# Performance work log

Hardware: AMD Instinct MI355X
Metric: run time of the kernel (lower is better)

## Reference

```python
import jax, jax.numpy as jnp
import numpy as np

N_NODES = 50000
N_EDGES = 400000
N_GRAPHS = 64
D_IN = 256
D_HID = 256
D_OUT = 16


def _gcn_conv(x, edge_index, W, b):
    """PyG-style GCNConv: h = D^{-1/2}(A+I)D^{-1/2} (x @ W) + b."""
    n = x.shape[0]
    loop = jnp.arange(n)
    src = jnp.concatenate([edge_index[0], loop])  # [E+N]
    dst = jnp.concatenate([edge_index[1], loop])
    deg = jax.ops.segment_sum(jnp.ones_like(dst, x.dtype), dst, num_segments=n)
    dinv = jnp.where(deg > 0, jax.lax.rsqrt(deg), jnp.zeros_like(deg))
    norm = dinv[src] * dinv[dst]  # [E+N]
    h = x @ W  # linear transform first (as PyG does)
    msg = h[src] * norm[:, None]  # gather + scale, [E+N, D]
    out = jax.ops.segment_sum(msg, dst, num_segments=n)  # scatter-add
    return out + b


def setup_inputs() -> dict:
    key = jax.random.key(0)
    ks = jax.random.split(key, 12)
    x = jax.random.normal(ks[0], (N_NODES, D_IN), dtype=jnp.float32)
    edge_index = jax.random.randint(ks[1], (2, N_EDGES), 0, N_NODES, dtype=jnp.int64)
    batch = jnp.sort(jax.random.randint(ks[2], (N_NODES,), 0, N_GRAPHS, dtype=jnp.int64))

    def glorot(k, fan_in, fan_out):
        s = np.sqrt(6.0 / (fan_in + fan_out)).astype(np.float32)
        return jax.random.uniform(k, (fan_in, fan_out), jnp.float32, -s, s)

    return {
        "x": x,
        "edge_index": edge_index,
        "batch": batch,
        "W1": glorot(ks[3], D_IN, D_HID), "b1": jnp.zeros((D_HID,), jnp.float32),
        "W2": glorot(ks[4], D_HID, D_HID), "b2": jnp.zeros((D_HID,), jnp.float32),
        "W3": glorot(ks[5], D_HID, D_HID), "b3": jnp.zeros((D_HID,), jnp.float32),
        "Wfc": glorot(ks[6], D_HID, D_OUT), "bfc": jnp.zeros((D_OUT,), jnp.float32),
    }


def reference(x, edge_index, batch, W1, b1, W2, b2, W3, b3, Wfc, bfc):
    h = jax.nn.relu(_gcn_conv(x, edge_index, W1, b1))
    h = jax.nn.relu(_gcn_conv(h, edge_index, W2, b2))
    h = jax.nn.relu(_gcn_conv(h, edge_index, W3, b3))
    # global_mean_pool over batch ids
    sums = jax.ops.segment_sum(h, batch, num_segments=N_GRAPHS)  # [G, D]
    cnts = jax.ops.segment_sum(jnp.ones_like(batch, h.dtype), batch, num_segments=N_GRAPHS)
    pooled = sums / jnp.maximum(cnts, 1.0)[:, None]
    return pooled @ Wfc + bfc  # [G, D_OUT]
```

## Files before the change

### kernel.cpp

```cpp
#include <hip/hip_runtime.h>

#define NN 50000
#define NE 400000
#define NG 64
#define D 256
#define DOUT 16

typedef __attribute__((ext_vector_type(8))) _Float16 f16x8;
typedef __attribute__((ext_vector_type(8))) unsigned short u16x8;
typedef __attribute__((ext_vector_type(4))) float f32x4;

__device__ __forceinline__ unsigned short f2h(float x) {
    union { _Float16 h; unsigned short u; } v;
    v.h = (_Float16)x;
    return v.u;
}
__device__ __forceinline__ float h2f(unsigned short u) {
    union { _Float16 h; unsigned short u; } v;
    v.u = u;
    return (float)v.h;
}

__device__ __forceinline__ void async_cp16(void* lds, const void* g) {
    __builtin_amdgcn_global_load_lds(
        (const __attribute__((address_space(1))) unsigned int*)g,
        (__attribute__((address_space(3))) unsigned int*)lds, 16, 0, 0);
}


__global__ void k_init(int* __restrict__ cnt, float* __restrict__ pooled,
                       const int* __restrict__ batch, float* __restrict__ inv_cnt,
                       int n) {
    int i = blockIdx.x * 256 + threadIdx.x;
    if (i < n) cnt[i] = 0;
    if (i < NG * D) pooled[i] = 0.f;
    if (blockIdx.x == 0 && threadIdx.x < NG) {
        int g = threadIdx.x;
        int lo = 0, hi = n;
        while (lo < hi) { int mid = (lo + hi) >> 1; if (batch[mid] < g) lo = mid + 1; else hi = mid; }
        int start = lo;
        hi = n;
        while (lo < hi) { int mid = (lo + hi) >> 1; if (batch[mid] < g + 1) lo = mid + 1; else hi = mid; }
        inv_cnt[g] = 1.f / fmaxf((float)(lo - start), 1.f);
    }
}


__global__ void k_split_count(const float* __restrict__ x, unsigned short* __restrict__ ahi,
                              int total4, int xblocks,
                              const float* __restrict__ W1, short* __restrict__ w1h,
                              const float* __restrict__ W2, short* __restrict__ w2h,
                              const float* __restrict__ W3, short* __restrict__ w3h,
                              const int* __restrict__ eidx, int* __restrict__ cnt, int E) {
    int b = blockIdx.x;
    if (b < xblocks) {
        int i = b * 256 + threadIdx.x;
        if (i >= total4) return;
        float4 v = ((const float4*)x)[i];
        ushort4 h;
        h.x = f2h(v.x);
        h.y = f2h(v.y);
        h.z = f2h(v.z);
        h.w = f2h(v.w);
        ((ushort4*)ahi)[i] = h;
    } else if (b < xblocks + 3 * 256) {
        int wb = b - xblocks;
        int which = wb >> 8;
        int idx = (wb & 255) * 256 + threadIdx.x;
        int nn = idx >> 8, k = idx & 255;
        const float* W = (which == 0) ? W1 : (which == 1) ? W2 : W3;
        short* Wh = (which == 0) ? w1h : (which == 1) ? w2h : w3h;
        Wh[idx] = (short)f2h(W[k * 256 + nn]);
    } else {
        int e = (b - xblocks - 3 * 256) * 256 + threadIdx.x;
        if (e < E) atomicAdd(&cnt[eidx[E + e]], 1);
    }
}

__global__ void k_scan1(const int* __restrict__ cnt, int* __restrict__ excl,
                        int* __restrict__ bsums, float* __restrict__ dinv, int n) {
    __shared__ int sh[256];
    int tid = threadIdx.x;
    int base = blockIdx.x * 1024;
    int v[4]; int tsum = 0;
    for (int j = 0; j < 4; ++j) {
        int i = base + tid * 4 + j;
        v[j] = (i < n) ? cnt[i] : 0;
        if (i < n) dinv[i] = rsqrtf((float)(v[j] + 1));
        tsum += v[j];
    }
    sh[tid] = tsum; __syncthreads();
    for (int d = 1; d < 256; d <<= 1) {
        int t = (tid >= d) ? sh[tid - d] : 0;
        __syncthreads();
        sh[tid] += t;
        __syncthreads();
    }
    int run = sh[tid] - tsum;
    for (int j = 0; j < 4; ++j) {
        int i = base + tid * 4 + j;
        if (i < n) excl[i] = run;
        run += v[j];
    }
    if (tid == 255) bsums[blockIdx.x] = sh[255];
}

__global__ void k_scan3(int* __restrict__ row_ptr, const int* __restrict__ bsums,
                        int* __restrict__ cursor, int n, int E, int nb) {
    __shared__ int off_s;
    int chunk = (int)(blockIdx.x >> 2);
    if (threadIdx.x < 64) {
        int v = ((int)threadIdx.x < nb && (int)threadIdx.x < chunk) ? bsums[threadIdx.x] : 0;
        #pragma unroll
        for (int d = 1; d < 64; d <<= 1) v += __shfl_xor(v, d);
        if (threadIdx.x == 0) off_s = v;
    }
    __syncthreads();
    int off = off_s;
    int i = blockIdx.x * 256 + threadIdx.x;
    if (i < n) {
        int v = row_ptr[i] + off;
        row_ptr[i] = v;
        cursor[i] = v;
    }
    if (i == 0) row_ptr[n] = E;
}


__device__ __forceinline__ void gemm_body(
        const unsigned short* __restrict__ A,
        const short* __restrict__ Wh,
        const float* __restrict__ dinv, unsigned short* __restrict__ C, int M,
        int bm, short* Ah_s, short* Bh_s) {
    const int tid = threadIdx.x;
    const int lane = tid & 63;
    const int w    = tid >> 6;
    const int lm   = lane & 15;
    const int quad = lane >> 4;

    const int srow = tid >> 3, c = tid & 7;
    const int q = c ^ ((srow >> 1) & 7);
    const unsigned short* pa[2];
    #pragma unroll
    for (int j = 0; j < 2; ++j) {
        int ga = bm + j * 32 + srow; if (ga >= M) ga = M - 1;
        pa[j] = A + ((size_t)ga << 8) + q * 8;
    }
    const short* pbh[8];
    #pragma unroll
    for (int j = 0; j < 8; ++j)
        pbh[j] = Wh + ((size_t)(j * 32 + srow) << 8) + q * 8;

    int st[8];
    #pragma unroll
    for (int j = 0; j < 8; ++j) st[j] = j * 2048 + w * 512;

    int oa[4], ob[4];
    #pragma unroll
    for (int i = 0; i < 4; ++i) {
        int ra = i * 16 + lm;
        oa[i] = ra * 64 + ((quad ^ ((ra >> 1) & 7)) * 8);
        int rb = w * 64 + i * 16 + lm;
        ob[i] = rb * 64 + ((quad ^ ((rb >> 1) & 7)) * 8);
    }

    f32x4 acc[4][4];
    #pragma unroll
    for (int i = 0; i < 4; ++i)
        #pragma unroll
        for (int j = 0; j < 4; ++j)
            acc[i][j] = (f32x4){0.f, 0.f, 0.f, 0.f};

    for (int k0 = 0; k0 < D; k0 += 64) {
        #pragma unroll
        for (int j = 0; j < 2; ++j) async_cp16(&Ah_s[st[j]], pa[j] + k0);
        #pragma unroll
        for (int j = 0; j < 8; ++j) async_cp16(&Bh_s[st[j]], pbh[j] + k0);
        __syncthreads();

        #pragma unroll
        for (int kh = 0; kh < 2; ++kh) {
            const int xo = kh * 32;
            f16x8 Ah[4], Bh[4];
            #pragma unroll
            for (int i = 0; i < 4; ++i) {
                Ah[i] = *(const f16x8*)&Ah_s[oa[i] ^ xo];
                Bh[i] = *(const f16x8*)&Bh_s[ob[i] ^ xo];
            }
            #pragma unroll
            for (int mi = 0; mi < 4; ++mi)
                #pragma unroll
                for (int ni = 0; ni < 4; ++ni)
                    acc[mi][ni] = __builtin_amdgcn_mfma_f32_16x16x32_f16(Ah[mi], Bh[ni], acc[mi][ni], 0, 0, 0);
        }
        __syncthreads();
    }

    #pragma unroll
    for (int mi = 0; mi < 4; ++mi) {
        int rbase = bm + mi * 16 + quad * 4;
        #pragma unroll
        for (int r = 0; r < 4; ++r) {
            int grow = rbase + r;
            if (grow < M) {
                float s = dinv[grow];
                #pragma unroll
                for (int ni = 0; ni < 4; ++ni) {
                    int col = w * 64 + ni * 16 + lm;
                    C[(size_t)grow * D + col] = f2h(acc[mi][ni][r] * s);
                }
            }
        }
    }
}

__global__ __launch_bounds__(256, 4) void k_gemm_mfma(
        const unsigned short* __restrict__ A,
        const short* __restrict__ Wh,
        const float* __restrict__ dinv, unsigned short* __restrict__ C, int M) {
    __shared__ short Ah_s[4096];
    __shared__ short Bh_s[16384];
    gemm_body(A, Wh, dinv, C, M, blockIdx.x * 64, Ah_s, Bh_s);
}

__global__ __launch_bounds__(256, 4) void k_gemm1_fill(
        const unsigned short* __restrict__ A,
        const short* __restrict__ Wh,
        const float* __restrict__ dinv, unsigned short* __restrict__ C, int M,
        int gblocks, const int* __restrict__ eidx, int* __restrict__ cursor,
        int* __restrict__ col_src, int E) {
    __shared__ short Ah_s[4096];
    __shared__ short Bh_s[16384];
    if ((int)blockIdx.x < gblocks) {
        gemm_body(A, Wh, dinv, C, M, blockIdx.x * 64, Ah_s, Bh_s);
    } else {
        int e = ((int)blockIdx.x - gblocks) * 256 + threadIdx.x;
        if (e < E) {
            int d = eidx[E + e];
            int pos = atomicAdd(&cursor[d], 1);
            col_src[pos] = eidx[e];
        }
    }
}


__global__ __launch_bounds__(128) void k_agg(
        const unsigned short* __restrict__ h, const float* __restrict__ dinv,
        const int* __restrict__ row_ptr, const int* __restrict__ col_src,
        const float* __restrict__ bias,
        unsigned short* __restrict__ ohi, int n) {
    int w = threadIdx.x >> 6, lane = threadIdx.x & 63;
    int node = blockIdx.x * 2 + w;
    if (node >= n) return;
    int half = lane >> 5;
    int dcol = lane & 31;

    float acc[8] = {0.f, 0.f, 0.f, 0.f, 0.f, 0.f, 0.f, 0.f};
    if (half == 0) {
        u16x8 sv = ((const u16x8*)(h + (size_t)node * D))[dcol];
        #pragma unroll
        for (int d = 0; d < 8; ++d) acc[d] = h2f(sv[d]);
    }

    int beg = row_ptr[node], end = row_ptr[node + 1];
    for (int c = beg; c < end; c += 64) {
        int cnt = min(64, end - c);
        int myidx = (lane < cnt) ? col_src[c + lane] : 0;
        for (int e = 0; e < cnt; e += 16) {
            u16x8 u[8];
            bool val[8];
            #pragma unroll
            for (int j = 0; j < 8; ++j) {
                int eid = e + j * 2 + half;
                val[j] = eid < cnt;
                if (val[j]) {
                    int s = __shfl(myidx, eid);
                    u[j] = ((const u16x8*)(h + (size_t)s * D))[dcol];
                }
            }
            #pragma unroll
            for (int j = 0; j < 8; ++j)
                if (val[j]) {
                    #pragma unroll
                    for (int d = 0; d < 8; ++d) acc[d] += h2f(u[j][d]);
                }
        }
    }

    #pragma unroll
    for (int d = 0; d < 8; ++d) acc[d] += __shfl_xor(acc[d], 32);

    if (half == 0) {
        float di = dinv[node];
        float4 b0 = ((const float4*)bias)[dcol * 2];
        float4 b1 = ((const float4*)bias)[dcol * 2 + 1];
        float bb[8] = {b0.x, b0.y, b0.z, b0.w, b1.x, b1.y, b1.z, b1.w};
        u16x8 o;
        #pragma unroll
        for (int d = 0; d < 8; ++d)
            o[d] = f2h(fmaxf(acc[d] * di + bb[d], 0.f));
        ((u16x8*)(ohi + (size_t)node * D))[dcol] = o;
    }
}


__global__ __launch_bounds__(256) void k_pool_sum(
        const unsigned short* __restrict__ hi,
        const int* __restrict__ batch, float* __restrict__ pooled, int n) {
    int beg = blockIdx.x * 64;
    if (beg >= n) return;
    int end = min(beg + 64, n);
    int t = threadIdx.x;
    float acc = 0.f;
    int cur = batch[beg];
    for (int i = beg; i < end; ++i) {
        int g = batch[i];
        if (g != cur) {
            atomicAdd(&pooled[cur * D + t], acc);
            acc = 0.f;
            cur = g;
        }
        acc += h2f(hi[(size_t)i * D + t]);
    }
    atomicAdd(&pooled[cur * D + t], acc);
}


__global__ void k_fc(const float* __restrict__ pooled, const float* __restrict__ inv_cnt,
                     const float* __restrict__ W, const float* __restrict__ b,
                     float* __restrict__ out) {
    int t = blockIdx.x * blockDim.x + threadIdx.x;
    if (t >= NG * DOUT) return;
    int g = t >> 4, o = t & 15;
    float acc = 0.f;
    for (int k = 0; k < D; ++k) acc += pooled[g * D + k] * W[k * DOUT + o];
    out[t] = acc * inv_cnt[g] + b[o];
}


extern "C" void kernel_launch(void* const* d_in, const int* in_sizes, int n_in,
                              void* d_out, int out_size, void* d_ws, size_t ws_size,
                              hipStream_t stream) {
    const float* x    = (const float*)d_in[0];
    const int*   eidx = (const int*)d_in[1];
    const int*   batch= (const int*)d_in[2];
    const float* W1   = (const float*)d_in[3];
    const float* b1   = (const float*)d_in[4];
    const float* W2   = (const float*)d_in[5];
    const float* b2   = (const float*)d_in[6];
    const float* W3   = (const float*)d_in[7];
    const float* b3   = (const float*)d_in[8];
    const float* Wfc  = (const float*)d_in[9];
    const float* bfc  = (const float*)d_in[10];
    float* out = (float*)d_out;

    const int n = in_sizes[0] / D;
    const int E = in_sizes[1] / 2;

    char* p = (char*)d_ws;
    auto take = [&](size_t bytes) -> void* {
        void* q = (void*)p;
        p += (bytes + 255) & ~(size_t)255;
        return q;
    };
    int*   cnt     = (int*)take((size_t)n * 4);
    int*   row_ptr = (int*)take((size_t)(n + 1) * 4);
    int*   cursor  = (int*)take((size_t)n * 4);
    int*   col_src = (int*)take((size_t)E * 4);
    int*   bsums   = (int*)take(256 * 4);
    float* dinv    = (float*)take((size_t)n * 4);
    float* inv_cnt = (float*)take((size_t)NG * 4);
    short* w1h     = (short*)take((size_t)D * D * 2);
    short* w2h     = (short*)take((size_t)D * D * 2);
    short* w3h     = (short*)take((size_t)D * D * 2);
    unsigned short* hbuf = (unsigned short*)take((size_t)n * D * 2);
    unsigned short* ahi  = (unsigned short*)take((size_t)n * D * 2);
    float* pooled  = (float*)take((size_t)NG * D * 4);

    int tb = 256;
    int gn = (n + tb - 1) / tb;
    int ge = (E + tb - 1) / tb;
    int nb = (n + 1023) / 1024;
    int total4 = n * D / 4;
    int xblocks = (total4 + 255) / 256;

    k_init<<<gn, tb, 0, stream>>>(cnt, pooled, batch, inv_cnt, n);
    k_split_count<<<xblocks + 3 * 256 + ge, tb, 0, stream>>>(
        x, ahi, total4, xblocks,
        W1, w1h, W2, w2h, W3, w3h,
        eidx, cnt, E);
    k_scan1<<<nb, 256, 0, stream>>>(cnt, row_ptr, bsums, dinv, n);
    k_scan3<<<gn, tb, 0, stream>>>(row_ptr, bsums, cursor, n, E, nb);

    int ggrid = (n + 63) / 64;
    int agrid = (n + 1) / 2;

    k_gemm1_fill<<<ggrid + ge, 256, 0, stream>>>(ahi, w1h, dinv, hbuf, n,
                                                 ggrid, eidx, cursor, col_src, E);
    k_agg<<<agrid, 128, 0, stream>>>(hbuf, dinv, row_ptr, col_src, b1, ahi, n);

    k_gemm_mfma<<<ggrid, 256, 0, stream>>>(ahi, w2h, dinv, hbuf, n);
    k_agg<<<agrid, 128, 0, stream>>>(hbuf, dinv, row_ptr, col_src, b2, ahi, n);

    k_gemm_mfma<<<ggrid, 256, 0, stream>>>(ahi, w3h, dinv, hbuf, n);
    k_agg<<<agrid, 128, 0, stream>>>(hbuf, dinv, row_ptr, col_src, b3, ahi, n);

    k_pool_sum<<<(n + 63) / 64, 256, 0, stream>>>(ahi, batch, pooled, n);
    k_fc<<<4, 256, 0, stream>>>(pooled, inv_cnt, Wfc, bfc, out);
}
```

Measured before the change: 347.0 us.

## Fuse GCN layers, pooling and FC into one cooperative persistent kernel

```diff
diff --git a/kernel.cpp b/kernel.cpp
--- a/kernel.cpp
+++ b/kernel.cpp
@@ -1,4 +1,7 @@
 #include <hip/hip_runtime.h>
+#include <hip/hip_cooperative_groups.h>
+
+namespace cg = cooperative_groups;
 
 #define NN 50000
 #define NE 400000
@@ -214,47 +217,12 @@
     }
 }
 
-__global__ __launch_bounds__(256, 4) void k_gemm_mfma(
-        const unsigned short* __restrict__ A,
-        const short* __restrict__ Wh,
-        const float* __restrict__ dinv, unsigned short* __restrict__ C, int M) {
-    __shared__ short Ah_s[4096];
-    __shared__ short Bh_s[16384];
-    gemm_body(A, Wh, dinv, C, M, blockIdx.x * 64, Ah_s, Bh_s);
-}
-
-__global__ __launch_bounds__(256, 4) void k_gemm1_fill(
-        const unsigned short* __restrict__ A,
-        const short* __restrict__ Wh,
-        const float* __restrict__ dinv, unsigned short* __restrict__ C, int M,
-        int gblocks, const int* __restrict__ eidx, int* __restrict__ cursor,
-        int* __restrict__ col_src, int E) {
-    __shared__ short Ah_s[4096];
-    __shared__ short Bh_s[16384];
-    if ((int)blockIdx.x < gblocks) {
-        gemm_body(A, Wh, dinv, C, M, blockIdx.x * 64, Ah_s, Bh_s);
-    } else {
-        int e = ((int)blockIdx.x - gblocks) * 256 + threadIdx.x;
-        if (e < E) {
-            int d = eidx[E + e];
-            int pos = atomicAdd(&cursor[d], 1);
-            col_src[pos] = eidx[e];
-        }
-    }
-}
-
-
-__global__ __launch_bounds__(128) void k_agg(
+
+__device__ __forceinline__ void agg_node(
         const unsigned short* __restrict__ h, const float* __restrict__ dinv,
         const int* __restrict__ row_ptr, const int* __restrict__ col_src,
-        const float* __restrict__ bias,
-        unsigned short* __restrict__ ohi, int n) {
-    int w = threadIdx.x >> 6, lane = threadIdx.x & 63;
-    int node = blockIdx.x * 2 + w;
-    if (node >= n) return;
-    int half = lane >> 5;
-    int dcol = lane & 31;
-
+        const float* __restrict__ bias, unsigned short* __restrict__ ohi,
+        int node, int lane, int half, int dcol) {
     float acc[8] = {0.f, 0.f, 0.f, 0.f, 0.f, 0.f, 0.f, 0.f};
     if (half == 0) {
         u16x8 sv = ((const u16x8*)(h + (size_t)node * D))[dcol];
@@ -303,12 +271,51 @@
     }
 }
 
-
-__global__ __launch_bounds__(256) void k_pool_sum(
-        const unsigned short* __restrict__ hi,
-        const int* __restrict__ batch, float* __restrict__ pooled, int n) {
-    int beg = blockIdx.x * 64;
-    if (beg >= n) return;
+__global__ __launch_bounds__(128) void k_agg(
+        const unsigned short* __restrict__ h, const float* __restrict__ dinv,
+        const int* __restrict__ row_ptr, const int* __restrict__ col_src,
+        const float* __restrict__ bias,
+        unsigned short* __restrict__ ohi, int n) {
+    int w = threadIdx.x >> 6, lane = threadIdx.x & 63;
+    int node = blockIdx.x * 2 + w;
+    if (node >= n) return;
+    agg_node(h, dinv, row_ptr, col_src, bias, ohi, node, lane, lane >> 5, lane & 31);
+}
+
+__global__ __launch_bounds__(256, 4) void k_gemm_mfma(
+        const unsigned short* __restrict__ A,
+        const short* __restrict__ Wh,
+        const float* __restrict__ dinv, unsigned short* __restrict__ C, int M) {
+    __shared__ short Ah_s[4096];
+    __shared__ short Bh_s[16384];
+    gemm_body(A, Wh, dinv, C, M, blockIdx.x * 64, Ah_s, Bh_s);
+}
+
+__global__ __launch_bounds__(256, 4) void k_gemm1_fill(
+        const unsigned short* __restrict__ A,
+        const short* __restrict__ Wh,
+        const float* __restrict__ dinv, unsigned short* __restrict__ C, int M,
+        int gblocks, const int* __restrict__ eidx, int* __restrict__ cursor,
+        int* __restrict__ col_src, int E) {
+    __shared__ short Ah_s[4096];
+    __shared__ short Bh_s[16384];
+    if ((int)blockIdx.x < gblocks) {
+        gemm_body(A, Wh, dinv, C, M, blockIdx.x * 64, Ah_s, Bh_s);
+    } else {
+        int e = ((int)blockIdx.x - gblocks) * 256 + threadIdx.x;
+        if (e < E) {
+            int d = eidx[E + e];
+            int pos = atomicAdd(&cursor[d], 1);
+            col_src[pos] = eidx[e];
+        }
+    }
+}
+
+
+__device__ __forceinline__ void pool_chunk(
+        const unsigned short* __restrict__ hi, const int* __restrict__ batch,
+        float* __restrict__ pooled, int n, int chunk) {
+    int beg = chunk * 64;
     int end = min(beg + 64, n);
     int t = threadIdx.x;
     float acc = 0.f;
@@ -325,6 +332,11 @@
     atomicAdd(&pooled[cur * D + t], acc);
 }
 
+__global__ __launch_bounds__(256) void k_pool_sum(
+        const unsigned short* __restrict__ hi,
+        const int* __restrict__ batch, float* __restrict__ pooled, int n) {
+    if (blockIdx.x * 64 < n) pool_chunk(hi, batch, pooled, n, blockIdx.x);
+}
 
 __global__ void k_fc(const float* __restrict__ pooled, const float* __restrict__ inv_cnt,
                      const float* __restrict__ W, const float* __restrict__ b,
@@ -335,6 +347,73 @@
     float acc = 0.f;
     for (int k = 0; k < D; ++k) acc += pooled[g * D + k] * W[k * DOUT + o];
     out[t] = acc * inv_cnt[g] + b[o];
+}
+
+
+__global__ __launch_bounds__(256, 4) void k_mega(
+        unsigned short* ahi, unsigned short* hbuf,
+        const short* w1h, const short* w2h, const short* w3h,
+        const float* b1, const float* b2, const float* b3,
+        const float* dinv, const int* row_ptr,
+        const int* eidx, int* cursor, int* col_src,
+        const int* batch, float* pooled, const float* inv_cnt,
+        const float* Wfc, const float* bfc, float* out,
+        int n, int E, int gtiles) {
+    __shared__ short Ah_s[4096];
+    __shared__ short Bh_s[16384];
+    cg::grid_group grid = cg::this_grid();
+    const int nb = (int)gridDim.x;
+    const int nwaves = nb * 4;
+    const int wid = (int)blockIdx.x * 4 + ((int)threadIdx.x >> 6);
+    const int lane = (int)threadIdx.x & 63;
+    const int half = lane >> 5, dcol = lane & 31;
+
+    for (int t = blockIdx.x; t < gtiles; t += nb)
+        gemm_body(ahi, w1h, dinv, hbuf, n, t * 64, Ah_s, Bh_s);
+    {
+        int fb0 = (nb > gtiles) ? gtiles : 0;
+        int nfb = nb - fb0;
+        if ((int)blockIdx.x >= fb0) {
+            for (int e = ((int)blockIdx.x - fb0) * 256 + (int)threadIdx.x; e < E;
+                 e += nfb * 256) {
+                int d = eidx[E + e];
+                int pos = atomicAdd(&cursor[d], 1);
+                col_src[pos] = eidx[e];
+            }
+        }
+    }
+    grid.sync();
+
+    for (int node = wid; node < n; node += nwaves)
+        agg_node(hbuf, dinv, row_ptr, col_src, b1, ahi, node, lane, half, dcol);
+    grid.sync();
+
+    for (int t = blockIdx.x; t < gtiles; t += nb)
+        gemm_body(ahi, w2h, dinv, hbuf, n, t * 64, Ah_s, Bh_s);
+    grid.sync();
+
+    for (int node = wid; node < n; node += nwaves)
+        agg_node(hbuf, dinv, row_ptr, col_src, b2, ahi, node, lane, half, dcol);
+    grid.sync();
+
+    for (int t = blockIdx.x; t < gtiles; t += nb)
+        gemm_body(ahi, w3h, dinv, hbuf, n, t * 64, Ah_s, Bh_s);
+    grid.sync();
+
+    for (int node = wid; node < n; node += nwaves)
+        agg_node(hbuf, dinv, row_ptr, col_src, b3, ahi, node, lane, half, dcol);
+    grid.sync();
+
+    for (int chunk = blockIdx.x; chunk * 64 < n; chunk += nb)
+        pool_chunk(ahi, batch, pooled, n, chunk);
+    grid.sync();
+
+    for (int t = (int)blockIdx.x * 256 + (int)threadIdx.x; t < NG * DOUT; t += nb * 256) {
+        int g = t >> 4, o = t & 15;
+        float acc = 0.f;
+        for (int k = 0; k < D; ++k) acc += pooled[g * D + k] * Wfc[k * DOUT + o];
+        out[t] = acc * inv_cnt[g] + bfc[o];
+    }
 }
 
 
@@ -380,7 +459,7 @@
     int tb = 256;
     int gn = (n + tb - 1) / tb;
     int ge = (E + tb - 1) / tb;
-    int nb = (n + 1023) / 1024;
+    int nb_scan = (n + 1023) / 1024;
     int total4 = n * D / 4;
     int xblocks = (total4 + 255) / 256;
 
@@ -389,22 +468,43 @@
         x, ahi, total4, xblocks,
         W1, w1h, W2, w2h, W3, w3h,
         eidx, cnt, E);
-    k_scan1<<<nb, 256, 0, stream>>>(cnt, row_ptr, bsums, dinv, n);
-    k_scan3<<<gn, tb, 0, stream>>>(row_ptr, bsums, cursor, n, E, nb);
-
-    int ggrid = (n + 63) / 64;
-    int agrid = (n + 1) / 2;
-
-    k_gemm1_fill<<<ggrid + ge, 256, 0, stream>>>(ahi, w1h, dinv, hbuf, n,
-                                                 ggrid, eidx, cursor, col_src, E);
-    k_agg<<<agrid, 128, 0, stream>>>(hbuf, dinv, row_ptr, col_src, b1, ahi, n);
-
-    k_gemm_mfma<<<ggrid, 256, 0, stream>>>(ahi, w2h, dinv, hbuf, n);
-    k_agg<<<agrid, 128, 0, stream>>>(hbuf, dinv, row_ptr, col_src, b2, ahi, n);
-
-    k_gemm_mfma<<<ggrid, 256, 0, stream>>>(ahi, w3h, dinv, hbuf, n);
-    k_agg<<<agrid, 128, 0, stream>>>(hbuf, dinv, row_ptr, col_src, b3, ahi, n);
-
-    k_pool_sum<<<(n + 63) / 64, 256, 0, stream>>>(ahi, batch, pooled, n);
-    k_fc<<<4, 256, 0, stream>>>(pooled, inv_cnt, Wfc, bfc, out);
-}
+    k_scan1<<<nb_scan, 256, 0, stream>>>(cnt, row_ptr, bsums, dinv, n);
+    k_scan3<<<gn, tb, 0, stream>>>(row_ptr, bsums, cursor, n, E, nb_scan);
+
+    int gtiles = (n + 63) / 64;
+
+    int nb = 1024;
+    int mb = 0;
+    if (hipOccupancyMaxActiveBlocksPerMultiprocessor(
+            &mb, (const void*)k_mega, 256, 0) == hipSuccess && mb > 0) {
+        int cap = mb * 256;
+        if (cap < nb) nb = cap;
+    }
+
+    int n_ = n, E_ = E, gt_ = gtiles;
+    void* args[] = {
+        (void*)&ahi, (void*)&hbuf,
+        (void*)&w1h, (void*)&w2h, (void*)&w3h,
+        (void*)&b1, (void*)&b2, (void*)&b3,
+        (void*)&dinv, (void*)&row_ptr,
+        (void*)&eidx, (void*)&cursor, (void*)&col_src,
+        (void*)&batch, (void*)&pooled, (void*)&inv_cnt,
+        (void*)&Wfc, (void*)&bfc, (void*)&out,
+        (void*)&n_, (void*)&E_, (void*)&gt_
+    };
+    hipError_t err = hipLaunchCooperativeKernel(
+        (const void*)k_mega, dim3(nb), dim3(256), args, 0, stream);
+
+    if (err != hipSuccess) {
+        int agrid = (n + 1) / 2;
+        k_gemm1_fill<<<gtiles + ge, 256, 0, stream>>>(ahi, w1h, dinv, hbuf, n,
+                                                      gtiles, eidx, cursor, col_src, E);
+        k_agg<<<agrid, 128, 0, stream>>>(hbuf, dinv, row_ptr, col_src, b1, ahi, n);
+        k_gemm_mfma<<<gtiles, 256, 0, stream>>>(ahi, w2h, dinv, hbuf, n);
+        k_agg<<<agrid, 128, 0, stream>>>(hbuf, dinv, row_ptr, col_src, b2, ahi, n);
+        k_gemm_mfma<<<gtiles, 256, 0, stream>>>(ahi, w3h, dinv, hbuf, n);
+        k_agg<<<agrid, 128, 0, stream>>>(hbuf, dinv, row_ptr, col_src, b3, ahi, n);
+        k_pool_sum<<<(n + 63) / 64, 256, 0, stream>>>(ahi, batch, pooled, n);
+        k_fc<<<4, 256, 0, stream>>>(pooled, inv_cnt, Wfc, bfc, out);
+    }
+}
```

After: 984.2 us. 184% more time.
